# Optimization experiments

Hardware: AMD Instinct MI355X
Metric: run time of the kernel (lower is better)

Reference implementation:

```python
import jax, jax.numpy as jnp
import numpy as np

N_NODES = 32768
N_EDGES = 262144
HEAD = 8
CHANNEL = 64
LAYER_NUM = 2
HC = HEAD * CHANNEL  # 512


def setup_inputs() -> dict:
    key = jax.random.key(0)
    ks = jax.random.split(key, 12)
    def lin(k, fan_in, fan_out):
        s = 1.0 / np.sqrt(fan_in)
        kw, kb = jax.random.split(k)
        W = jax.random.uniform(kw, (fan_in, fan_out), jnp.float32, -s, s)
        b = jax.random.uniform(kb, (fan_out,), jnp.float32, -s, s)
        return W, b
    Wn, bn = lin(ks[0], 118, HC)
    We, be = lin(ks[1], 22, HC)
    Wa, ba = lin(ks[2], 2 * HC, HC)
    attn_w = jax.random.normal(ks[3], (1, HEAD, CHANNEL), jnp.float32) * 0.1
    x = jax.random.normal(ks[4], (N_NODES, 118), jnp.float32)
    edge_feat = jax.random.normal(ks[5], (N_EDGES, 22), jnp.float32)
    src = jax.random.randint(ks[6], (N_EDGES,), 0, N_NODES)
    dst = jax.random.randint(ks[7], (N_EDGES,), 0, N_NODES)
    return {"x": x, "edge_feat": edge_feat, "src": src, "dst": dst,
            "Wn": Wn, "bn": bn, "We": We, "be": be, "Wa": Wa, "ba": ba,
            "attn_w": attn_w}


def reference(x, edge_feat, src, dst, Wn, bn, We, be, Wa, ba, attn_w):
    N = x.shape[0]
    H, C = attn_w.shape[1], attn_w.shape[2]
    h = x @ Wn + bn                      # [N, H*C]
    _eh = edge_feat @ We + be            # computed in original forward, never used
    for _ in range(LAYER_NUM):
        # gather src/dst node states onto edges and score them (GATv2 style)
        e = jnp.concatenate([h[src], h[dst]], axis=-1)            # [E, 2HC]
        e = jax.nn.leaky_relu(e @ Wa + ba, negative_slope=0.01)   # [E, HC]
        score = jnp.sum(e.reshape(-1, H, C) * attn_w, axis=-1)    # [E, H]
        # edge softmax normalized over incoming edges of each dst node
        m = jax.ops.segment_max(score, dst, num_segments=N)       # [N, H]
        ex = jnp.exp(score - m[dst])                              # [E, H]
        denom = jax.ops.segment_sum(ex, dst, num_segments=N)      # [N, H]
        alpha = ex / denom[dst]                                   # [E, H]
        # weighted message passing: u_mul_e then sum over dst
        msg = h[src].reshape(-1, H, C) * alpha[:, :, None]        # [E, H, C]
        h = jax.ops.segment_sum(msg, dst, num_segments=N).reshape(N, H * C)
    return h
```

## Files before the change

kernel.cpp:

```cpp
#include <hip/hip_runtime.h>
#include <hip/hip_bf16.h>
#include <stdint.h>

#define N_NODES 32768
#define N_EDGES 262144

typedef __attribute__((ext_vector_type(8))) short short8;
typedef __attribute__((ext_vector_type(4))) float f32x4;
typedef __attribute__((ext_vector_type(4))) uint u32x4;

typedef const __attribute__((address_space(1))) void* gvp;
typedef __attribute__((address_space(3))) void* lvp;

__device__ __forceinline__ float bf2f(ushort u) {
  return __uint_as_float(((uint)u) << 16);
}
__device__ __forceinline__ ushort f2bf(float f) {
  uint x = __float_as_uint(f);
  uint r = (x + 0x7fffu + ((x >> 16) & 1u)) >> 16;
  return (ushort)r;
}
__device__ __forceinline__ float loadf(const void* p, size_t i, int isbf) {
  return isbf ? bf2f(((const ushort*)p)[i]) : ((const float*)p)[i];
}

__global__ void detect_dtype(const uint* __restrict__ xw, int* __restrict__ flag) {
  __shared__ int cnt;
  if (threadIdx.x == 0) cnt = 0;
  __syncthreads();
  int good = 0;
  for (int i = threadIdx.x; i < 1024; i += 256) {
    uint lo = xw[i] & 0xFFFFu;
    uint ef = (lo >> 7) & 0xFFu;
    if (lo == 0u || (ef >= 0x60u && ef <= 0x90u)) good++;
  }
  atomicAdd(&cnt, good);
  __syncthreads();
  if (threadIdx.x == 0) *flag = (cnt >= 614) ? 1 : 0;
}

__global__ void prep_all(const void* __restrict__ Wa, const void* __restrict__ Wn,
                         const void* __restrict__ ba, const void* __restrict__ bn,
                         const void* __restrict__ aw, const void* __restrict__ x,
                         const int* __restrict__ flag,
                         ushort* __restrict__ W2T, ushort* __restrict__ WnpT,
                         ushort* __restrict__ Wn_pad, float* __restrict__ bias2,
                         float* __restrict__ bnf, float* __restrict__ wf,
                         float* __restrict__ zbias, ushort* __restrict__ xp) {
  const int fl = *flag;
  const int b = blockIdx.x;
  if (b < 2048) {
    int t = b * 256 + threadIdx.x;
    int n = t >> 9, k = t & 511;
    size_t idx = (n < 512) ? ((size_t)k * 512 + n) : ((size_t)(512 + k) * 512 + (n - 512));
    W2T[t] = f2bf(loadf(Wa, idx, fl));
  } else if (b < 2304) {
    int t = (b - 2048) * 256 + threadIdx.x;
    int n = t >> 7, k = t & 127;
    WnpT[t] = (k < 118) ? f2bf(loadf(Wn, (size_t)k * 512 + n, fl)) : (ushort)0;
  } else if (b < 2560) {
    int t = (b - 2304) * 256 + threadIdx.x;
    int n = t >> 9, j = t & 511;
    Wn_pad[t] = (n < 118) ? f2bf(loadf(Wn, (size_t)n * 512 + j, fl)) : (ushort)0;
  } else if (b < 2564) {
    int t = (b - 2560) * 256 + threadIdx.x;
    if (t < 1024) bias2[t] = (t < 512) ? loadf(ba, t, fl) : 0.f;
    if (t < 512) { bnf[t] = loadf(bn, t, fl); wf[t] = loadf(aw, t, fl); }
    if (t < 128) zbias[t] = 0.f;
  } else {
    int t = (b - 2564) * 256 + threadIdx.x;
    int i = t >> 7, k = t & 127;
    xp[t] = (k < 118) ? f2bf(loadf(x, (size_t)i * 118 + k, fl)) : (ushort)0;
  }
}

__global__ __launch_bounds__(256)
void build_bc(const ushort* __restrict__ W2T, const float* __restrict__ bnf,
              const float* __restrict__ bias2, float* __restrict__ bc) {
  const int wave = threadIdx.x >> 6, lane = threadIdx.x & 63;
  const int j = blockIdx.x * 4 + wave;
  const uint4 v = *(const uint4*)(W2T + (size_t)j * 512 + lane * 8);
  const float4 b0 = *(const float4*)(bnf + lane * 8);
  const float4 b1 = *(const float4*)(bnf + lane * 8 + 4);
  const uint w[4] = {v.x, v.y, v.z, v.w};
  const float bb[8] = {b0.x, b0.y, b0.z, b0.w, b1.x, b1.y, b1.z, b1.w};
  float s = 0.f;
#pragma unroll
  for (int i = 0; i < 4; ++i) {
    s += __uint_as_float(w[i] << 16) * bb[2 * i];
    s += __uint_as_float(w[i] & 0xffff0000u) * bb[2 * i + 1];
  }
  s += __shfl_xor(s, 1);  s += __shfl_xor(s, 2);  s += __shfl_xor(s, 4);
  s += __shfl_xor(s, 8);  s += __shfl_xor(s, 16); s += __shfl_xor(s, 32);
  if (lane == 0) bc[j] = s + bias2[j];
}

__global__ void csr_count(const int* __restrict__ dst, int* __restrict__ cnt) {
  int e = blockIdx.x * blockDim.x + threadIdx.x;
  atomicAdd(&cnt[dst[e]], 1);
}

__global__ __launch_bounds__(1024)
void csr_scan(const int* __restrict__ cnt, int* __restrict__ rowptr,
              int* __restrict__ cursor) {
  __shared__ int part[1024];
  const int t = threadIdx.x;
  const int base = t * 32;
  int loc[32];
  int s = 0;
#pragma unroll
  for (int i = 0; i < 32; ++i) { loc[i] = s; s += cnt[base + i]; }
  part[t] = s;
  __syncthreads();
  for (int off = 1; off < 1024; off <<= 1) {
    int v = (t >= off) ? part[t - off] : 0;
    __syncthreads();
    part[t] += v;
    __syncthreads();
  }
  int pre = (t == 0) ? 0 : part[t - 1];
#pragma unroll
  for (int i = 0; i < 32; ++i) {
    int v = pre + loc[i];
    rowptr[base + i] = v;
    cursor[base + i] = v;
  }
  if (t == 1023) rowptr[N_NODES] = part[1023];
}

__global__ void csr_fill(const int* __restrict__ dst, const int* __restrict__ src,
                         int* __restrict__ cursor, int* __restrict__ esrc) {
  int e = blockIdx.x * blockDim.x + threadIdx.x;
  int p = atomicAdd(&cursor[dst[e]], 1);
  esrc[p] = src[e];
}

__global__ __launch_bounds__(256)
void gemm_bf16(const ushort* __restrict__ A, const ushort* __restrict__ BT,
               const float* __restrict__ bias, ushort* __restrict__ C,
               int M, int N, int K) {
  __shared__ __align__(16) ushort As[128 * 32];
  __shared__ __align__(16) ushort Bs[128 * 32];
  const int tid = threadIdx.x, wave = tid >> 6, lane = tid & 63;
  const int bm = blockIdx.y * 128, bn = blockIdx.x * 128;
  const int wm = (wave >> 1) * 64, wn = (wave & 1) * 64;
  const int fcol = lane & 15, quad = lane >> 4;

  const f32x4 zero = {0.f, 0.f, 0.f, 0.f};
  f32x4 acc[4][4];
#pragma unroll
  for (int i = 0; i < 4; ++i)
#pragma unroll
    for (int j = 0; j < 4; ++j) acc[i][j] = zero;

  for (int k0 = 0; k0 < K; k0 += 32) {
#pragma unroll
    for (int r = 0; r < 2; ++r) {
      int o = r * 4096 + wave * 1024 + lane * 16;
      int row = o >> 6;
      int ke = (o & 63) >> 1;
      const ushort* gA = A + (size_t)(bm + row) * K + k0 + ke;
      const ushort* gB = BT + (size_t)(bn + row) * K + k0 + ke;
      ushort* lA = As + ((r * 4096 + wave * 1024) >> 1);
      ushort* lB = Bs + ((r * 4096 + wave * 1024) >> 1);
      __builtin_amdgcn_global_load_lds((gvp)(const void*)gA, (lvp)(void*)lA, 16, 0, 0);
      __builtin_amdgcn_global_load_lds((gvp)(const void*)gB, (lvp)(void*)lB, 16, 0, 0);
    }
    __syncthreads();
    short8 a[4], b[4];
#pragma unroll
    for (int i = 0; i < 4; ++i) {
      a[i] = *(const short8*)&As[(wm + i * 16 + fcol) * 32 + quad * 8];
      b[i] = *(const short8*)&Bs[(wn + i * 16 + fcol) * 32 + quad * 8];
    }
#pragma unroll
    for (int i = 0; i < 4; ++i)
#pragma unroll
      for (int j = 0; j < 4; ++j)
        acc[i][j] = __builtin_amdgcn_mfma_f32_16x16x32_bf16(a[i], b[j], acc[i][j], 0, 0, 0);
    __syncthreads();
  }

#pragma unroll
  for (int i = 0; i < 4; ++i) {
    int rowb = bm + wm + i * 16 + quad * 4;
#pragma unroll
    for (int j = 0; j < 4; ++j) {
      int col = bn + wn + j * 16 + fcol;
      float bb = bias[col];
#pragma unroll
      for (int r = 0; r < 4; ++r) {
        C[(size_t)(rowb + r) * N + col] = f2bf(acc[i][j][r] + bb);
      }
    }
  }
}

__global__ __launch_bounds__(256)
void node_fused(const ushort* __restrict__ PQ, const ushort* __restrict__ hb_in,
                const int* __restrict__ esrc, const int* __restrict__ rowptr,
                const float* __restrict__ wf, const int* __restrict__ flag,
                ushort* __restrict__ hb_out, void* __restrict__ out, int write_out) {
  const int wave = threadIdx.x >> 6, lane = threadIdx.x & 63;
  const int d = blockIdx.x * 4 + wave;
  const int beg = rowptr[d], end = rowptr[d + 1];
  const int c0 = lane * 8;

  const uint4 qv = *(const uint4*)(PQ + (size_t)d * 1024 + 512 + c0);
  const uint qw[4] = {qv.x, qv.y, qv.z, qv.w};
  float q[8], w[8];
#pragma unroll
  for (int i = 0; i < 4; ++i) {
    q[2 * i]     = __uint_as_float(qw[i] << 16);
    q[2 * i + 1] = __uint_as_float(qw[i] & 0xffff0000u);
  }
  const float4 w0 = *(const float4*)(wf + c0);
  const float4 w1 = *(const float4*)(wf + c0 + 4);
  w[0] = w0.x; w[1] = w0.y; w[2] = w0.z; w[3] = w0.w;
  w[4] = w1.x; w[5] = w1.y; w[6] = w1.z; w[7] = w1.w;

  float m = -3e38f, den = 0.f;
  float acc[8] = {0.f, 0.f, 0.f, 0.f, 0.f, 0.f, 0.f, 0.f};

  if (beg < end) {
    const int last = end - 1;
    const int s0 = esrc[beg];
    int sN = esrc[(beg + 1 <= last) ? beg + 1 : last];
    uint4 pv0 = *(const uint4*)(PQ + (size_t)s0 * 1024 + c0);
    uint4 hv0 = *(const uint4*)(hb_in + (size_t)s0 * 512 + c0);

    for (int j = beg; j < end; ++j) {
      const int s2 = esrc[(j + 2 <= last) ? j + 2 : last];
      uint4 pv1 = pv0, hv1 = hv0;
      if (j < last) {
        pv1 = *(const uint4*)(PQ + (size_t)sN * 1024 + c0);
        hv1 = *(const uint4*)(hb_in + (size_t)sN * 512 + c0);
      }

      const uint pw[4] = {pv0.x, pv0.y, pv0.z, pv0.w};
      const uint hw[4] = {hv0.x, hv0.y, hv0.z, hv0.w};
      float t = 0.f;
#pragma unroll
      for (int i = 0; i < 4; ++i) {
        float ea = __uint_as_float(pw[i] << 16) + q[2 * i];
        float eb = __uint_as_float(pw[i] & 0xffff0000u) + q[2 * i + 1];
        ea = (ea > 0.f) ? ea : 0.01f * ea;
        eb = (eb > 0.f) ? eb : 0.01f * eb;
        t += ea * w[2 * i] + eb * w[2 * i + 1];
      }
      t += __shfl_xor(t, 1);
      t += __shfl_xor(t, 2);
      t += __shfl_xor(t, 4);
      if (__any(t > m)) {
        const float mnew = fmaxf(m, t);
        const float corr = __expf(m - mnew);
        const float ex = __expf(t - mnew);
        den = den * corr + ex;
#pragma unroll
        for (int i = 0; i < 4; ++i) {
          acc[2 * i]     = acc[2 * i] * corr     + ex * __uint_as_float(hw[i] << 16);
          acc[2 * i + 1] = acc[2 * i + 1] * corr + ex * __uint_as_float(hw[i] & 0xffff0000u);
        }
        m = mnew;
      } else {
        const float ex = __expf(t - m);
        den += ex;
#pragma unroll
        for (int i = 0; i < 4; ++i) {
          acc[2 * i]     += ex * __uint_as_float(hw[i] << 16);
          acc[2 * i + 1] += ex * __uint_as_float(hw[i] & 0xffff0000u);
        }
      }
      pv0 = pv1; hv0 = hv1; sN = s2;
    }
  }

  const float inv = (end > beg) ? (1.f / den) : 0.f;
  uint o[4];
#pragma unroll
  for (int i = 0; i < 4; ++i) {
    float v0 = acc[2 * i] * inv, v1 = acc[2 * i + 1] * inv;
    o[i] = (uint)f2bf(v0) | ((uint)f2bf(v1) << 16);
  }
  u32x4 ov = {o[0], o[1], o[2], o[3]};
  *(u32x4*)(hb_out + (size_t)d * 512 + c0) = ov;
  if (write_out) {
    if (*flag) {
      __builtin_nontemporal_store(ov, (u32x4*)((ushort*)out + (size_t)d * 512 + c0));
    } else {
      f32x4 f0 = {acc[0] * inv, acc[1] * inv, acc[2] * inv, acc[3] * inv};
      f32x4 f1 = {acc[4] * inv, acc[5] * inv, acc[6] * inv, acc[7] * inv};
      __builtin_nontemporal_store(f0, (f32x4*)((float*)out + (size_t)d * 512 + c0));
      __builtin_nontemporal_store(f1, (f32x4*)((float*)out + (size_t)d * 512 + c0 + 4));
    }
  }
}

extern "C" void kernel_launch(void* const* d_in, const int* in_sizes, int n_in,
                              void* d_out, int out_size, void* d_ws, size_t ws_size,
                              hipStream_t stream) {
  const void* x   = d_in[0];
  const int*  src = (const int*)d_in[2];
  const int*  dst = (const int*)d_in[3];
  const void* Wn  = d_in[4];
  const void* bn  = d_in[5];
  const void* Wa  = d_in[8];
  const void* ba  = d_in[9];
  const void* aw  = d_in[10];

  char* ws = (char*)d_ws;
  size_t off = 0;
  auto alloc = [&](size_t bytes) {
    char* p = ws + off;
    off = (off + bytes + 255) & ~(size_t)255;
    return p;
  };
  ushort* hbA    = (ushort*)alloc((size_t)N_NODES * 512 * 2);
  ushort* hbB    = (ushort*)alloc((size_t)N_NODES * 512 * 2);
  ushort* PQ     = (ushort*)alloc((size_t)N_NODES * 1024 * 2);
  int*    esrc   = (int*)   alloc((size_t)N_EDGES * 4);
  int*    rowptr = (int*)   alloc((size_t)(N_NODES + 1) * 4);
  int*    cnt    = (int*)   alloc((size_t)N_NODES * 4);
  int*    cursor = (int*)   alloc((size_t)N_NODES * 4);
  ushort* W2T    = (ushort*)alloc((size_t)1024 * 512 * 2);
  ushort* WcT    = (ushort*)alloc((size_t)1024 * 128 * 2);
  ushort* Wn_pad = (ushort*)alloc((size_t)128 * 512 * 2);
  float*  bias2  = (float*) alloc(1024 * 4);
  float*  bc     = (float*) alloc(1024 * 4);
  float*  zbias  = (float*) alloc(128 * 4);
  ushort* xp     = (ushort*)alloc((size_t)N_NODES * 128 * 2);
  ushort* WnpT   = (ushort*)alloc((size_t)512 * 128 * 2);
  float*  bnf    = (float*) alloc(512 * 4);
  float*  wf     = (float*) alloc(512 * 4);
  int*    flag   = (int*)   alloc(256);

  detect_dtype<<<1, 256, 0, stream>>>((const uint*)x, flag);
  prep_all<<<2564 + (N_NODES * 128) / 256, 256, 0, stream>>>(
      Wa, Wn, ba, bn, aw, x, flag, W2T, WnpT, Wn_pad, bias2, bnf, wf, zbias, xp);
  build_bc<<<256, 256, 0, stream>>>(W2T, bnf, bias2, bc);
  {
    dim3 g(128 / 128, 1024 / 128);
    gemm_bf16<<<g, 256, 0, stream>>>(W2T, Wn_pad, zbias, WcT, 1024, 128, 512);
  }

  hipMemsetAsync(cnt, 0, (size_t)N_NODES * 4, stream);
  csr_count<<<N_EDGES / 256, 256, 0, stream>>>(dst, cnt);
  csr_scan<<<1, 1024, 0, stream>>>(cnt, rowptr, cursor);
  csr_fill<<<N_EDGES / 256, 256, 0, stream>>>(dst, src, cursor, esrc);

  {
    dim3 g(512 / 128, N_NODES / 128);
    gemm_bf16<<<g, 256, 0, stream>>>(xp, WnpT, bnf, hbA, N_NODES, 512, 128);
  }

  {
    dim3 g(1024 / 128, N_NODES / 128);
    gemm_bf16<<<g, 256, 0, stream>>>(xp, WcT, bc, PQ, N_NODES, 1024, 128);
  }
  node_fused<<<N_NODES / 4, 256, 0, stream>>>(PQ, hbA, esrc, rowptr, wf, flag,
                                              hbB, d_out, 0);

  {
    dim3 g(1024 / 128, N_NODES / 128);
    gemm_bf16<<<g, 256, 0, stream>>>(hbB, W2T, bias2, PQ, N_NODES, 1024, 512);
  }
  node_fused<<<N_NODES / 4, 256, 0, stream>>>(PQ, hbB, esrc, rowptr, wf, flag,
                                              hbA, d_out, 1);
}
```

Before: 462.1 us.

## Fold layer-2 projection into layer-1 aggregation via linearity of weighted sums

Because the layer-2 projection is linear and the softmax weights sum to one, the layer-1 kernel now also accumulates attention-weighted sums of the layer-1 P and Q rows, producing layer-2 PQ directly. This removes the N×1024×512 GEMM between the two layers. The cost is three gathers per edge instead of two, plus an extra 64 MB PQ2 buffer. Separately, the edge-count atomics are merged into the prep kernel as extra blocks, and the node kernel's software prefetch of the next edge's rows is dropped in favour of a simpler loop; the final layer also skips the unused hb_out write.

```diff
diff --git a/kernel.cpp b/kernel.cpp
--- a/kernel.cpp
+++ b/kernel.cpp
@@ -42,13 +42,19 @@
 __global__ void prep_all(const void* __restrict__ Wa, const void* __restrict__ Wn,
                          const void* __restrict__ ba, const void* __restrict__ bn,
                          const void* __restrict__ aw, const void* __restrict__ x,
-                         const int* __restrict__ flag,
+                         const int* __restrict__ flag, const int* __restrict__ dst,
                          ushort* __restrict__ W2T, ushort* __restrict__ WnpT,
                          ushort* __restrict__ Wn_pad, float* __restrict__ bias2,
                          float* __restrict__ bnf, float* __restrict__ wf,
-                         float* __restrict__ zbias, ushort* __restrict__ xp) {
+                         float* __restrict__ zbias, ushort* __restrict__ xp,
+                         int* __restrict__ cnt) {
+  const int b = blockIdx.x;
+  if (b >= 2564 + 16384) {
+    int e = (b - 2564 - 16384) * 256 + threadIdx.x;
+    atomicAdd(&cnt[dst[e]], 1);
+    return;
+  }
   const int fl = *flag;
-  const int b = blockIdx.x;
   if (b < 2048) {
     int t = b * 256 + threadIdx.x;
     int n = t >> 9, k = t & 511;
@@ -95,11 +101,6 @@
   if (lane == 0) bc[j] = s + bias2[j];
 }
 
-__global__ void csr_count(const int* __restrict__ dst, int* __restrict__ cnt) {
-  int e = blockIdx.x * blockDim.x + threadIdx.x;
-  atomicAdd(&cnt[dst[e]], 1);
-}
-
 __global__ __launch_bounds__(1024)
 void csr_scan(const int* __restrict__ cnt, int* __restrict__ rowptr,
               int* __restrict__ cursor) {
@@ -197,6 +198,113 @@
 }
 
 __global__ __launch_bounds__(256)
+void node_fused_l1(const ushort* __restrict__ PQ1, const ushort* __restrict__ h0,
+                   const int* __restrict__ esrc, const int* __restrict__ rowptr,
+                   const float* __restrict__ wf, const float* __restrict__ bias2,
+                   ushort* __restrict__ h1, ushort* __restrict__ PQ2) {
+  const int wave = threadIdx.x >> 6, lane = threadIdx.x & 63;
+  const int d = blockIdx.x * 4 + wave;
+  const int beg = rowptr[d], end = rowptr[d + 1];
+  const int c0 = lane * 8;
+
+  const uint4 qv = *(const uint4*)(PQ1 + (size_t)d * 1024 + 512 + c0);
+  const uint qw[4] = {qv.x, qv.y, qv.z, qv.w};
+  float q[8], w[8];
+#pragma unroll
+  for (int i = 0; i < 4; ++i) {
+    q[2 * i]     = __uint_as_float(qw[i] << 16);
+    q[2 * i + 1] = __uint_as_float(qw[i] & 0xffff0000u);
+  }
+  const float4 w0 = *(const float4*)(wf + c0);
+  const float4 w1 = *(const float4*)(wf + c0 + 4);
+  w[0] = w0.x; w[1] = w0.y; w[2] = w0.z; w[3] = w0.w;
+  w[4] = w1.x; w[5] = w1.y; w[6] = w1.z; w[7] = w1.w;
+
+  float m = -3e38f, den = 0.f;
+  float aP[8], aQ[8], aH[8];
+#pragma unroll
+  for (int i = 0; i < 8; ++i) { aP[i] = 0.f; aQ[i] = 0.f; aH[i] = 0.f; }
+
+  if (beg < end) {
+    int sj = esrc[beg];
+    for (int j = beg; j < end; ++j) {
+      const int s = sj;
+      if (j + 1 < end) sj = esrc[j + 1];
+      const uint4 pa = *(const uint4*)(PQ1 + (size_t)s * 1024 + c0);
+      const uint4 pb = *(const uint4*)(PQ1 + (size_t)s * 1024 + 512 + c0);
+      const uint4 hv = *(const uint4*)(h0 + (size_t)s * 512 + c0);
+      const uint paw[4] = {pa.x, pa.y, pa.z, pa.w};
+      const uint pbw[4] = {pb.x, pb.y, pb.z, pb.w};
+      const uint hw[4]  = {hv.x, hv.y, hv.z, hv.w};
+      float t = 0.f;
+#pragma unroll
+      for (int i = 0; i < 4; ++i) {
+        float ea = __uint_as_float(paw[i] << 16) + q[2 * i];
+        float eb = __uint_as_float(paw[i] & 0xffff0000u) + q[2 * i + 1];
+        ea = (ea > 0.f) ? ea : 0.01f * ea;
+        eb = (eb > 0.f) ? eb : 0.01f * eb;
+        t += ea * w[2 * i] + eb * w[2 * i + 1];
+      }
+      t += __shfl_xor(t, 1);
+      t += __shfl_xor(t, 2);
+      t += __shfl_xor(t, 4);
+      if (__any(t > m)) {
+        const float mnew = fmaxf(m, t);
+        const float corr = __expf(m - mnew);
+        const float ex = __expf(t - mnew);
+        den = den * corr + ex;
+#pragma unroll
+        for (int i = 0; i < 4; ++i) {
+          aP[2 * i]     = aP[2 * i] * corr     + ex * __uint_as_float(paw[i] << 16);
+          aP[2 * i + 1] = aP[2 * i + 1] * corr + ex * __uint_as_float(paw[i] & 0xffff0000u);
+          aQ[2 * i]     = aQ[2 * i] * corr     + ex * __uint_as_float(pbw[i] << 16);
+          aQ[2 * i + 1] = aQ[2 * i + 1] * corr + ex * __uint_as_float(pbw[i] & 0xffff0000u);
+          aH[2 * i]     = aH[2 * i] * corr     + ex * __uint_as_float(hw[i] << 16);
+          aH[2 * i + 1] = aH[2 * i + 1] * corr + ex * __uint_as_float(hw[i] & 0xffff0000u);
+        }
+        m = mnew;
+      } else {
+        const float ex = __expf(t - m);
+        den += ex;
+#pragma unroll
+        for (int i = 0; i < 4; ++i) {
+          aP[2 * i]     += ex * __uint_as_float(paw[i] << 16);
+          aP[2 * i + 1] += ex * __uint_as_float(paw[i] & 0xffff0000u);
+          aQ[2 * i]     += ex * __uint_as_float(pbw[i] << 16);
+          aQ[2 * i + 1] += ex * __uint_as_float(pbw[i] & 0xffff0000u);
+          aH[2 * i]     += ex * __uint_as_float(hw[i] << 16);
+          aH[2 * i + 1] += ex * __uint_as_float(hw[i] & 0xffff0000u);
+        }
+      }
+    }
+  }
+
+  const int deg = end - beg;
+  const float inv = deg ? (1.f / den) : 0.f;
+  const float4 bp0 = *(const float4*)(bias2 + c0);
+  const float4 bp1 = *(const float4*)(bias2 + c0 + 4);
+  const float bp[8] = {bp0.x, bp0.y, bp0.z, bp0.w, bp1.x, bp1.y, bp1.z, bp1.w};
+  uint oP[4], oQ[4], oH[4];
+#pragma unroll
+  for (int i = 0; i < 4; ++i) {
+    float p0 = deg ? aP[2 * i] * inv : bp[2 * i];
+    float p1 = deg ? aP[2 * i + 1] * inv : bp[2 * i + 1];
+    float q0 = deg ? aQ[2 * i] * inv : 0.f;
+    float q1 = deg ? aQ[2 * i + 1] * inv : 0.f;
+    float h0v = aH[2 * i] * inv, h1v = aH[2 * i + 1] * inv;
+    oP[i] = (uint)f2bf(p0) | ((uint)f2bf(p1) << 16);
+    oQ[i] = (uint)f2bf(q0) | ((uint)f2bf(q1) << 16);
+    oH[i] = (uint)f2bf(h0v) | ((uint)f2bf(h1v) << 16);
+  }
+  u32x4 vP = {oP[0], oP[1], oP[2], oP[3]};
+  u32x4 vQ = {oQ[0], oQ[1], oQ[2], oQ[3]};
+  u32x4 vH = {oH[0], oH[1], oH[2], oH[3]};
+  *(u32x4*)(PQ2 + (size_t)d * 1024 + c0) = vP;
+  *(u32x4*)(PQ2 + (size_t)d * 1024 + 512 + c0) = vQ;
+  *(u32x4*)(h1 + (size_t)d * 512 + c0) = vH;
+}
+
+__global__ __launch_bounds__(256)
 void node_fused(const ushort* __restrict__ PQ, const ushort* __restrict__ hb_in,
                 const int* __restrict__ esrc, const int* __restrict__ rowptr,
                 const float* __restrict__ wf, const int* __restrict__ flag,
@@ -223,22 +331,14 @@
   float acc[8] = {0.f, 0.f, 0.f, 0.f, 0.f, 0.f, 0.f, 0.f};
 
   if (beg < end) {
-    const int last = end - 1;
-    const int s0 = esrc[beg];
-    int sN = esrc[(beg + 1 <= last) ? beg + 1 : last];
-    uint4 pv0 = *(const uint4*)(PQ + (size_t)s0 * 1024 + c0);
-    uint4 hv0 = *(const uint4*)(hb_in + (size_t)s0 * 512 + c0);
-
+    int sj = esrc[beg];
     for (int j = beg; j < end; ++j) {
-      const int s2 = esrc[(j + 2 <= last) ? j + 2 : last];
-      uint4 pv1 = pv0, hv1 = hv0;
-      if (j < last) {
-        pv1 = *(const uint4*)(PQ + (size_t)sN * 1024 + c0);
-        hv1 = *(const uint4*)(hb_in + (size_t)sN * 512 + c0);
-      }
-
-      const uint pw[4] = {pv0.x, pv0.y, pv0.z, pv0.w};
-      const uint hw[4] = {hv0.x, hv0.y, hv0.z, hv0.w};
+      const int s = sj;
+      if (j + 1 < end) sj = esrc[j + 1];
+      const uint4 pv = *(const uint4*)(PQ + (size_t)s * 1024 + c0);
+      const uint4 hv = *(const uint4*)(hb_in + (size_t)s * 512 + c0);
+      const uint pw[4] = {pv.x, pv.y, pv.z, pv.w};
+      const uint hw[4] = {hv.x, hv.y, hv.z, hv.w};
       float t = 0.f;
 #pragma unroll
       for (int i = 0; i < 4; ++i) {
@@ -271,7 +371,6 @@
           acc[2 * i + 1] += ex * __uint_as_float(hw[i] & 0xffff0000u);
         }
       }
-      pv0 = pv1; hv0 = hv1; sN = s2;
     }
   }
 
@@ -283,8 +382,9 @@
     o[i] = (uint)f2bf(v0) | ((uint)f2bf(v1) << 16);
   }
   u32x4 ov = {o[0], o[1], o[2], o[3]};
-  *(u32x4*)(hb_out + (size_t)d * 512 + c0) = ov;
-  if (write_out) {
+  if (!write_out) {
+    *(u32x4*)(hb_out + (size_t)d * 512 + c0) = ov;
+  } else {
     if (*flag) {
       __builtin_nontemporal_store(ov, (u32x4*)((ushort*)out + (size_t)d * 512 + c0));
     } else {
@@ -333,18 +433,19 @@
   float*  bnf    = (float*) alloc(512 * 4);
   float*  wf     = (float*) alloc(512 * 4);
   int*    flag   = (int*)   alloc(256);
+  ushort* PQ2    = (ushort*)alloc((size_t)N_NODES * 1024 * 2);
+  const bool fold = (off <= ws_size);
 
   detect_dtype<<<1, 256, 0, stream>>>((const uint*)x, flag);
-  prep_all<<<2564 + (N_NODES * 128) / 256, 256, 0, stream>>>(
-      Wa, Wn, ba, bn, aw, x, flag, W2T, WnpT, Wn_pad, bias2, bnf, wf, zbias, xp);
+  hipMemsetAsync(cnt, 0, (size_t)N_NODES * 4, stream);
+  prep_all<<<2564 + 16384 + 1024, 256, 0, stream>>>(
+      Wa, Wn, ba, bn, aw, x, flag, dst, W2T, WnpT, Wn_pad, bias2, bnf, wf, zbias,
+      xp, cnt);
   build_bc<<<256, 256, 0, stream>>>(W2T, bnf, bias2, bc);
   {
     dim3 g(128 / 128, 1024 / 128);
     gemm_bf16<<<g, 256, 0, stream>>>(W2T, Wn_pad, zbias, WcT, 1024, 128, 512);
   }
-
-  hipMemsetAsync(cnt, 0, (size_t)N_NODES * 4, stream);
-  csr_count<<<N_EDGES / 256, 256, 0, stream>>>(dst, cnt);
   csr_scan<<<1, 1024, 0, stream>>>(cnt, rowptr, cursor);
   csr_fill<<<N_EDGES / 256, 256, 0, stream>>>(dst, src, cursor, esrc);
 
@@ -352,18 +453,24 @@
     dim3 g(512 / 128, N_NODES / 128);
     gemm_bf16<<<g, 256, 0, stream>>>(xp, WnpT, bnf, hbA, N_NODES, 512, 128);
   }
-
   {
     dim3 g(1024 / 128, N_NODES / 128);
     gemm_bf16<<<g, 256, 0, stream>>>(xp, WcT, bc, PQ, N_NODES, 1024, 128);
   }
-  node_fused<<<N_NODES / 4, 256, 0, stream>>>(PQ, hbA, esrc, rowptr, wf, flag,
-                                              hbB, d_out, 0);
-
-  {
-    dim3 g(1024 / 128, N_NODES / 128);
-    gemm_bf16<<<g, 256, 0, stream>>>(hbB, W2T, bias2, PQ, N_NODES, 1024, 512);
-  }
-  node_fused<<<N_NODES / 4, 256, 0, stream>>>(PQ, hbB, esrc, rowptr, wf, flag,
-                                              hbA, d_out, 1);
-}
+
+  if (fold) {
+    node_fused_l1<<<N_NODES / 4, 256, 0, stream>>>(PQ, hbA, esrc, rowptr, wf,
+                                                   bias2, hbB, PQ2);
+    node_fused<<<N_NODES / 4, 256, 0, stream>>>(PQ2, hbB, esrc, rowptr, wf, flag,
+                                                hbA, d_out, 1);
+  } else {
+    node_fused<<<N_NODES / 4, 256, 0, stream>>>(PQ, hbA, esrc, rowptr, wf, flag,
+                                                hbB, d_out, 0);
+    {
+      dim3 g(1024 / 128, N_NODES / 128);
+      gemm_bf16<<<g, 256, 0, stream>>>(hbB, W2T, bias2, PQ, N_NODES, 1024, 512);
+    }
+    node_fused<<<N_NODES / 4, 256, 0, stream>>>(PQ, hbB, esrc, rowptr, wf, flag,
+                                                hbA, d_out, 1);
+  }
+}
```

Result: faster. 434.8 us (-5.9%).
